# Optimization experiments

Measured on AMD Instinct MI355X. Metric: run time of the kernel, lower is better.

## Reference

```python
import jax, jax.numpy as jnp
import numpy as np
import math

N_NODES = 100000
N_EDGES = 1600000
IN_DIM = 32
OUT_DIM = 32

def setup_inputs() -> dict:
    key = jax.random.key(0)
    k1, k2, k3, k4 = jax.random.split(key, 4)
    X = jax.random.normal(k1, (N_NODES, IN_DIM), dtype=jnp.float32)
    src_idx = jax.random.randint(k2, (N_EDGES,), 0, N_NODES, dtype=jnp.int64)
    dst_idx = jax.random.randint(k3, (N_EDGES,), 0, N_NODES, dtype=jnp.int64)
    # weights init: uniform(-stdv, stdv), stdv = 1/sqrt(output_dim)
    stdv = 1.0 / math.sqrt(OUT_DIM)
    W = jax.random.uniform(k4, (IN_DIM, OUT_DIM), dtype=jnp.float32,
                           minval=-stdv, maxval=stdv)
    return {"X": X, "W": W, "src_idx": src_idx, "dst_idx": dst_idx}

def reference(X, W, src_idx, dst_idx):
    # GIN sum-aggregation SpMM: agg[i] = sum_{j in N(i)} X[j]
    agg = jax.ops.segment_sum(X[src_idx], dst_idx, num_segments=N_NODES)
    # dense GEMM: X_prime = agg @ W
    return agg @ W
```

## Files before the change

### kernel.cpp

```cpp
#include <hip/hip_runtime.h>

#define N_DIM 32
#define NPB 64
#define NBINS_PAD 1600
#define CAPFINE 1280
#define CEPB 8192
#define EPT (CEPB / 512)
#define FT 512
#define GROWS 512

__device__ __forceinline__ unsigned f2bf_rne(float f) {
    unsigned u = __float_as_uint(f);
    return (u + 0x7FFFu + ((u >> 16) & 1u)) >> 16;
}
__device__ __forceinline__ float bf2f(unsigned h) {
    return __uint_as_float(h << 16);
}

__global__ __launch_bounds__(FT) void k_fused(const float* __restrict__ X,
                                              const float* __restrict__ W,
                                              unsigned* __restrict__ Y,
                                              const int* __restrict__ src,
                                              const int* __restrict__ dst,
                                              int* __restrict__ cursorF0,
                                              int* __restrict__ pairs,
                                              int n_nodes, int n_edges,
                                              int nb_fine, int nblk_g) {
    __shared__ int smem[8192 + 4096 + 2 * NBINS_PAD + 8];
    const int t = threadIdx.x;

    if (blockIdx.x < nblk_g) {
        float* Wlds = (float*)smem;
        for (int i = t; i < N_DIM * N_DIM; i += FT) Wlds[i] = W[i];
        __syncthreads();
        const int r = blockIdx.x * GROWS + t;
        if (r >= n_nodes) return;

        float x[N_DIM];
        const float4* xr = (const float4*)(X + (size_t)r * N_DIM);
#pragma unroll
        for (int i = 0; i < N_DIM / 4; ++i) {
            float4 v = xr[i];
            x[4 * i + 0] = v.x; x[4 * i + 1] = v.y;
            x[4 * i + 2] = v.z; x[4 * i + 3] = v.w;
        }
        float acc[N_DIM];
#pragma unroll
        for (int c = 0; c < N_DIM; ++c) acc[c] = 0.0f;
#pragma unroll
        for (int k = 0; k < N_DIM; ++k) {
            const float xk = x[k];
#pragma unroll
            for (int c = 0; c < N_DIM; ++c)
                acc[c] = fmaf(xk, Wlds[k * N_DIM + c], acc[c]);
        }
        unsigned yp[16];
#pragma unroll
        for (int q = 0; q < 16; ++q)
            yp[q] = f2bf_rne(acc[2 * q]) | (f2bf_rne(acc[2 * q + 1]) << 16);
        uint4* yr = (uint4*)(Y + (size_t)r * 16);
#pragma unroll
        for (int i = 0; i < 4; ++i)
            yr[i] = make_uint4(yp[4 * i], yp[4 * i + 1],
                               yp[4 * i + 2], yp[4 * i + 3]);
    } else {
        int* sortedV = smem;
        unsigned short* sortedB = (unsigned short*)(smem + 8192);
        int* off   = smem + 8192 + 4096;
        int* base2 = off + NBINS_PAD;
        int* misc  = base2 + NBINS_PAD;

        for (int i = t; i < nb_fine; i += FT) off[i] = 0;
        __syncthreads();
        const int start = (blockIdx.x - nblk_g) * CEPB;

        int vw[EPT], cw[EPT], rw[EPT];
#pragma unroll
        for (int k = 0; k < EPT; ++k) {
            int e = start + t + k * FT;
            if (e < n_edges) {
                int d = dst[e];
                cw[k] = d >> 6;
                vw[k] = src[e] | ((d & 63) << 17);
                rw[k] = atomicAdd(&off[cw[k]], 1);
            } else {
                cw[k] = -1;
            }
        }
        __syncthreads();

        if (t < 64) {
            int run = 0;
            for (int ch = 0; ch * 64 < nb_fine; ++ch) {
                int s = ch * 64 + t;
                int a = (s < nb_fine) ? off[s] : 0;
                int x = a;
#pragma unroll
                for (int o = 1; o < 64; o <<= 1) {
                    int u = __shfl_up(x, o, 64);
                    if (t >= o) x += u;
                }
                if (s < nb_fine) base2[s] = run + x - a;
                run += __shfl(x, 63, 64);
            }
            if (t == 0) misc[0] = run;
        }
        __syncthreads();

        for (int b = t; b < nb_fine; b += FT) {
            int c = off[b];
            int o = base2[b];
            int g = c ? atomicAdd(&cursorF0[b], c) : 0;
            off[b] = o;
            base2[b] = b * CAPFINE + g - o;
        }
        __syncthreads();

#pragma unroll
        for (int k = 0; k < EPT; ++k) {
            if (cw[k] >= 0) {
                int slot = off[cw[k]] + rw[k];
                sortedV[slot] = vw[k];
                sortedB[slot] = (unsigned short)cw[k];
            }
        }
        __syncthreads();

        const int total = misc[0];
        for (int i = t; i < total; i += FT) {
            int b = sortedB[i];
            int p = sortedV[i];
            int dest = base2[b] + i;
            if (dest - b * CAPFINE < CAPFINE) pairs[dest] = p;
        }
    }
}

__device__ __forceinline__ void addv(float* acc, uint4 v) {
    acc[0] += bf2f(v.x & 0xFFFFu); acc[1] += bf2f(v.x >> 16);
    acc[2] += bf2f(v.y & 0xFFFFu); acc[3] += bf2f(v.y >> 16);
    acc[4] += bf2f(v.z & 0xFFFFu); acc[5] += bf2f(v.z >> 16);
    acc[6] += bf2f(v.w & 0xFFFFu); acc[7] += bf2f(v.w >> 16);
}

__global__ __launch_bounds__(256) void k_agg(const uint4* __restrict__ Y4,
                                             const int* __restrict__ cursorF0,
                                             const int* __restrict__ pairs,
                                             float* __restrict__ out,
                                             int n_nodes) {
    __shared__ int sbin[CAPFINE];
    __shared__ int cnt[NPB];
    __shared__ int cst[NPB];
    __shared__ int excl[NPB];

    const int t = threadIdx.x;
    const int b = blockIdx.x;
    const int len = min(cursorF0[b], CAPFINE);
    const size_t segbase = (size_t)b * CAPFINE;
    const int g = t >> 2;
    const int l = t & 3;

    if (t < NPB) cnt[t] = 0;
    __syncthreads();

    int pv[CAPFINE / 256], rv[CAPFINE / 256];
#pragma unroll
    for (int k = 0; k < CAPFINE / 256; ++k) {
        int i = t + k * 256;
        if (i < len) {
            int p = pairs[segbase + i];
            pv[k] = p;
            rv[k] = atomicAdd(&cnt[p >> 17], 1);
        } else {
            pv[k] = -1;
        }
    }
    __syncthreads();
    if (t < 64) {
        int c0 = cnt[t];
        int c = c0;
#pragma unroll
        for (int off = 1; off < 64; off <<= 1) {
            int u = __shfl_up(c, off, 64);
            if (t >= off) c += u;
        }
        cst[t] = c;
        excl[t] = c - c0;
    }
    __syncthreads();
#pragma unroll
    for (int k = 0; k < CAPFINE / 256; ++k) {
        if (pv[k] >= 0) {
            int p = pv[k];
            sbin[excl[p >> 17] + rv[k]] = p & 0x1FFFF;
        }
    }
    __syncthreads();

    float acc[8];
#pragma unroll
    for (int i = 0; i < 8; ++i) acc[i] = 0.0f;

    const int s1 = cst[g];
    const int s0 = s1 - cnt[g];
    for (int e = s0; e < s1; e += 4) {
        const int m = s1 - e;
        int i0 = sbin[e];
        int i1 = sbin[e + ((m > 1) ? 1 : 0)];
        int i2 = sbin[e + ((m > 2) ? 2 : 0)];
        int i3 = sbin[e + ((m > 3) ? 3 : 0)];
        uint4 v0 = Y4[(size_t)i0 * 4 + l];
        uint4 v1 = Y4[(size_t)i1 * 4 + l];
        uint4 v2 = Y4[(size_t)i2 * 4 + l];
        uint4 v3 = Y4[(size_t)i3 * 4 + l];
        addv(acc, v0);
        if (m > 1) addv(acc, v1);
        if (m > 2) addv(acc, v2);
        if (m > 3) addv(acc, v3);
    }

    const int node = b * NPB + g;
    if (node < n_nodes) {
        ((float4*)out)[(size_t)node * 8 + 2 * l] =
            make_float4(acc[0], acc[1], acc[2], acc[3]);
        ((float4*)out)[(size_t)node * 8 + 2 * l + 1] =
            make_float4(acc[4], acc[5], acc[6], acc[7]);
    }
}

extern "C" void kernel_launch(void* const* d_in, const int* in_sizes, int n_in,
                              void* d_out, int out_size, void* d_ws, size_t ws_size,
                              hipStream_t stream) {
    const float* X   = (const float*)d_in[0];
    const float* W   = (const float*)d_in[1];
    const int*   src = (const int*)d_in[2];
    const int*   dst = (const int*)d_in[3];
    float* out = (float*)d_out;

    const int n_nodes = in_sizes[0] / N_DIM;
    const int n_edges = in_sizes[2];
    const int nb = (n_nodes + NPB - 1) / NPB;

    unsigned* Y   = (unsigned*)d_ws;
    int* cursorF0 = (int*)(Y + (size_t)n_nodes * 16);
    int* pairs    = cursorF0 + NBINS_PAD;

    const int nblk_g = (n_nodes + GROWS - 1) / GROWS;
    const int nblk_c = (n_edges + CEPB - 1) / CEPB;

    hipMemsetAsync(cursorF0, 0, (size_t)NBINS_PAD * sizeof(int), stream);

    k_fused<<<nblk_g + nblk_c, FT, 0, stream>>>(X, W, Y, src, dst, cursorF0, pairs,
                                                n_nodes, n_edges, nb, nblk_g);
    k_agg<<<nb, 256, 0, stream>>>((const uint4*)Y, cursorF0, pairs, out, n_nodes);
}
```

Baseline: 118.2 us.

## Double nodes per aggregation block and use two lanes per node

Bins now cover 128 destination nodes instead of 64, which halves the number of bins and aggregation blocks and doubles the per-bin capacity. In the aggregation kernel each node is handled by 2 threads with 16 accumulators each, not 4 threads with 8. The count scan is chunked to cover 128 counts. This aims to cut per-block overhead and atomic contention on the bin cursors, in exchange for fewer, heavier blocks and lower parallelism per node in the gather loop. The 7-bit local index still fits above the 17-bit source field.

```diff
diff --git a/kernel.cpp b/kernel.cpp
--- a/kernel.cpp
+++ b/kernel.cpp
@@ -1,9 +1,9 @@
 #include <hip/hip_runtime.h>
 
 #define N_DIM 32
-#define NPB 64
-#define NBINS_PAD 1600
-#define CAPFINE 1280
+#define NPB 128
+#define NBINS_PAD 800
+#define CAPFINE 2560
 #define CEPB 8192
 #define EPT (CEPB / 512)
 #define FT 512
@@ -80,8 +80,8 @@
             int e = start + t + k * FT;
             if (e < n_edges) {
                 int d = dst[e];
-                cw[k] = d >> 6;
-                vw[k] = src[e] | ((d & 63) << 17);
+                cw[k] = d >> 7;
+                vw[k] = src[e] | ((d & 127) << 17);
                 rw[k] = atomicAdd(&off[cw[k]], 1);
             } else {
                 cw[k] = -1;
@@ -157,8 +157,8 @@
     const int b = blockIdx.x;
     const int len = min(cursorF0[b], CAPFINE);
     const size_t segbase = (size_t)b * CAPFINE;
-    const int g = t >> 2;
-    const int l = t & 3;
+    const int g = t >> 1;
+    const int l = t & 1;
 
     if (t < NPB) cnt[t] = 0;
     __syncthreads();
@@ -177,15 +177,20 @@
     }
     __syncthreads();
     if (t < 64) {
-        int c0 = cnt[t];
-        int c = c0;
-#pragma unroll
-        for (int off = 1; off < 64; off <<= 1) {
-            int u = __shfl_up(c, off, 64);
-            if (t >= off) c += u;
-        }
-        cst[t] = c;
-        excl[t] = c - c0;
+        int run = 0;
+#pragma unroll
+        for (int ch = 0; ch < NPB / 64; ++ch) {
+            int c0 = cnt[ch * 64 + t];
+            int c = c0;
+#pragma unroll
+            for (int off = 1; off < 64; off <<= 1) {
+                int u = __shfl_up(c, off, 64);
+                if (t >= off) c += u;
+            }
+            cst[ch * 64 + t] = run + c;
+            excl[ch * 64 + t] = run + c - c0;
+            run += __shfl(c, 63, 64);
+        }
     }
     __syncthreads();
 #pragma unroll
@@ -197,9 +202,9 @@
     }
     __syncthreads();
 
-    float acc[8];
-#pragma unroll
-    for (int i = 0; i < 8; ++i) acc[i] = 0.0f;
+    float acc[16];
+#pragma unroll
+    for (int i = 0; i < 16; ++i) acc[i] = 0.0f;
 
     const int s1 = cst[g];
     const int s0 = s1 - cnt[g];
@@ -209,22 +214,27 @@
         int i1 = sbin[e + ((m > 1) ? 1 : 0)];
         int i2 = sbin[e + ((m > 2) ? 2 : 0)];
         int i3 = sbin[e + ((m > 3) ? 3 : 0)];
-        uint4 v0 = Y4[(size_t)i0 * 4 + l];
-        uint4 v1 = Y4[(size_t)i1 * 4 + l];
-        uint4 v2 = Y4[(size_t)i2 * 4 + l];
-        uint4 v3 = Y4[(size_t)i3 * 4 + l];
-        addv(acc, v0);
-        if (m > 1) addv(acc, v1);
-        if (m > 2) addv(acc, v2);
-        if (m > 3) addv(acc, v3);
+        uint4 v0a = Y4[(size_t)i0 * 4 + 2 * l];
+        uint4 v0b = Y4[(size_t)i0 * 4 + 2 * l + 1];
+        uint4 v1a = Y4[(size_t)i1 * 4 + 2 * l];
+        uint4 v1b = Y4[(size_t)i1 * 4 + 2 * l + 1];
+        uint4 v2a = Y4[(size_t)i2 * 4 + 2 * l];
+        uint4 v2b = Y4[(size_t)i2 * 4 + 2 * l + 1];
+        uint4 v3a = Y4[(size_t)i3 * 4 + 2 * l];
+        uint4 v3b = Y4[(size_t)i3 * 4 + 2 * l + 1];
+        addv(acc, v0a); addv(acc + 8, v0b);
+        if (m > 1) { addv(acc, v1a); addv(acc + 8, v1b); }
+        if (m > 2) { addv(acc, v2a); addv(acc + 8, v2b); }
+        if (m > 3) { addv(acc, v3a); addv(acc + 8, v3b); }
     }
 
     const int node = b * NPB + g;
     if (node < n_nodes) {
-        ((float4*)out)[(size_t)node * 8 + 2 * l] =
-            make_float4(acc[0], acc[1], acc[2], acc[3]);
-        ((float4*)out)[(size_t)node * 8 + 2 * l + 1] =
-            make_float4(acc[4], acc[5], acc[6], acc[7]);
+        float4* o4 = (float4*)out + (size_t)node * 8 + 4 * l;
+#pragma unroll
+        for (int i = 0; i < 4; ++i)
+            o4[i] = make_float4(acc[4 * i], acc[4 * i + 1],
+                                acc[4 * i + 2], acc[4 * i + 3]);
     }
 }
 
```

After: 120.0 us. Within noise of the previous version (+1.5%).

## Replace global atomic bin scatter with per-segment sorted chunks and offset tables

Applied to the files above, without the earlier changes.

Instead of atomically reserving space in global per-bin buckets and scattering pairs there, each edge-chunk block writes its locally sorted chunk contiguously, along with its per-bin offset table. The aggregation block then prefix-sums the per-segment counts for its bin and binary-searches the segments to gather its edges. This removes the memset, the global atomics and the scattered writes, at the cost of a 196-row offset read and a scan per aggregation block, plus a binary search per edge. It assumes nseg is at most 256.

```diff
diff --git a/kernel.cpp b/kernel.cpp
--- a/kernel.cpp
+++ b/kernel.cpp
@@ -6,6 +6,7 @@
 #define CAPFINE 1280
 #define CEPB 8192
 #define EPT (CEPB / 512)
+#define NSEG_MAX 256
 #define FT 512
 #define GROWS 512
 
@@ -22,11 +23,11 @@
                                               unsigned* __restrict__ Y,
                                               const int* __restrict__ src,
                                               const int* __restrict__ dst,
-                                              int* __restrict__ cursorF0,
-                                              int* __restrict__ pairs,
+                                              int* __restrict__ off2,
+                                              int* __restrict__ pairs2,
                                               int n_nodes, int n_edges,
                                               int nb_fine, int nblk_g) {
-    __shared__ int smem[8192 + 4096 + 2 * NBINS_PAD + 8];
+    __shared__ int smem[8192 + 2 * NBINS_PAD + 8];
     const int t = threadIdx.x;
 
     if (blockIdx.x < nblk_g) {
@@ -65,14 +66,14 @@
                                yp[4 * i + 2], yp[4 * i + 3]);
     } else {
         int* sortedV = smem;
-        unsigned short* sortedB = (unsigned short*)(smem + 8192);
-        int* off   = smem + 8192 + 4096;
-        int* base2 = off + NBINS_PAD;
-        int* misc  = base2 + NBINS_PAD;
+        int* off     = smem + 8192;
+        int* base2   = off + NBINS_PAD;
+        int* misc    = base2 + NBINS_PAD;
 
         for (int i = t; i < nb_fine; i += FT) off[i] = 0;
         __syncthreads();
-        const int start = (blockIdx.x - nblk_g) * CEPB;
+        const int seg = blockIdx.x - nblk_g;
+        const int start = seg * CEPB;
 
         int vw[EPT], cw[EPT], rw[EPT];
 #pragma unroll
@@ -107,32 +108,24 @@
         }
         __syncthreads();
 
+        int* myoff2 = off2 + (size_t)seg * NBINS_PAD;
         for (int b = t; b < nb_fine; b += FT) {
-            int c = off[b];
             int o = base2[b];
-            int g = c ? atomicAdd(&cursorF0[b], c) : 0;
+            myoff2[b] = o;
             off[b] = o;
-            base2[b] = b * CAPFINE + g - o;
-        }
-        __syncthreads();
-
-#pragma unroll
-        for (int k = 0; k < EPT; ++k) {
-            if (cw[k] >= 0) {
-                int slot = off[cw[k]] + rw[k];
-                sortedV[slot] = vw[k];
-                sortedB[slot] = (unsigned short)cw[k];
-            }
-        }
-        __syncthreads();
-
-        const int total = misc[0];
-        for (int i = t; i < total; i += FT) {
-            int b = sortedB[i];
-            int p = sortedV[i];
-            int dest = base2[b] + i;
-            if (dest - b * CAPFINE < CAPFINE) pairs[dest] = p;
-        }
+        }
+        if (t == 0) myoff2[nb_fine] = misc[0];
+        __syncthreads();
+
+#pragma unroll
+        for (int k = 0; k < EPT; ++k)
+            if (cw[k] >= 0)
+                sortedV[off[cw[k]] + rw[k]] = vw[k];
+        __syncthreads();
+
+        int4* d4 = (int4*)(pairs2 + (size_t)seg * CEPB);
+        const int4* s4 = (const int4*)sortedV;
+        for (int i = t; i < CEPB / 4; i += FT) d4[i] = s4[i];
     }
 }
 
@@ -144,31 +137,66 @@
 }
 
 __global__ __launch_bounds__(256) void k_agg(const uint4* __restrict__ Y4,
-                                             const int* __restrict__ cursorF0,
-                                             const int* __restrict__ pairs,
+                                             const int* __restrict__ off2,
+                                             const int* __restrict__ pairs2,
                                              float* __restrict__ out,
-                                             int n_nodes) {
+                                             int n_nodes, int nb_fine, int nseg) {
     __shared__ int sbin[CAPFINE];
+    __shared__ int sst[NSEG_MAX];
+    __shared__ int bnd[NSEG_MAX];
+    __shared__ int tlen;
     __shared__ int cnt[NPB];
     __shared__ int cst[NPB];
     __shared__ int excl[NPB];
 
     const int t = threadIdx.x;
     const int b = blockIdx.x;
-    const int len = min(cursorF0[b], CAPFINE);
-    const size_t segbase = (size_t)b * CAPFINE;
     const int g = t >> 2;
     const int l = t & 3;
 
+    if (t < NSEG_MAX) {
+        int s0v = 0, ln = 0;
+        if (t < nseg) {
+            const int* row = off2 + (size_t)t * NBINS_PAD;
+            s0v = row[b];
+            ln = row[b + 1] - s0v;
+        }
+        sst[t] = s0v;
+        bnd[t] = ln;
+    }
     if (t < NPB) cnt[t] = 0;
     __syncthreads();
+
+    if (t < 64) {
+        int run = 0;
+#pragma unroll
+        for (int ch = 0; ch < NSEG_MAX / 64; ++ch) {
+            int a = bnd[ch * 64 + t];
+            int x = a;
+#pragma unroll
+            for (int o = 1; o < 64; o <<= 1) {
+                int u = __shfl_up(x, o, 64);
+                if (t >= o) x += u;
+            }
+            bnd[ch * 64 + t] = run + x - a;
+            run += __shfl(x, 63, 64);
+        }
+        if (t == 0) tlen = run;
+    }
+    __syncthreads();
+    const int len = min(tlen, CAPFINE);
 
     int pv[CAPFINE / 256], rv[CAPFINE / 256];
 #pragma unroll
     for (int k = 0; k < CAPFINE / 256; ++k) {
         int i = t + k * 256;
         if (i < len) {
-            int p = pairs[segbase + i];
+            int lo = 0, hi = nseg - 1;
+            while (lo < hi) {
+                int mid = (lo + hi + 1) >> 1;
+                if (bnd[mid] <= i) lo = mid; else hi = mid - 1;
+            }
+            int p = pairs2[(size_t)lo * CEPB + sst[lo] + (i - bnd[lo])];
             pv[k] = p;
             rv[k] = atomicAdd(&cnt[p >> 17], 1);
         } else {
@@ -240,17 +268,16 @@
     const int n_nodes = in_sizes[0] / N_DIM;
     const int n_edges = in_sizes[2];
     const int nb = (n_nodes + NPB - 1) / NPB;
-
-    unsigned* Y   = (unsigned*)d_ws;
-    int* cursorF0 = (int*)(Y + (size_t)n_nodes * 16);
-    int* pairs    = cursorF0 + NBINS_PAD;
+    const int nseg = (n_edges + CEPB - 1) / CEPB;
+
+    unsigned* Y  = (unsigned*)d_ws;
+    int* off2    = (int*)(Y + (size_t)n_nodes * 16);
+    int* pairs2  = off2 + (size_t)nseg * NBINS_PAD;
 
     const int nblk_g = (n_nodes + GROWS - 1) / GROWS;
-    const int nblk_c = (n_edges + CEPB - 1) / CEPB;
-
-    hipMemsetAsync(cursorF0, 0, (size_t)NBINS_PAD * sizeof(int), stream);
-
-    k_fused<<<nblk_g + nblk_c, FT, 0, stream>>>(X, W, Y, src, dst, cursorF0, pairs,
-                                                n_nodes, n_edges, nb, nblk_g);
-    k_agg<<<nb, 256, 0, stream>>>((const uint4*)Y, cursorF0, pairs, out, n_nodes);
-}
+
+    k_fused<<<nblk_g + nseg, FT, 0, stream>>>(X, W, Y, src, dst, off2, pairs2,
+                                              n_nodes, n_edges, nb, nblk_g);
+    k_agg<<<nb, 256, 0, stream>>>((const uint4*)Y, off2, pairs2, out,
+                                  n_nodes, nb, nseg);
+}
```

After: 118.5 us. Within noise of the previous version (+0.2%).
